# Optimization experiments

Hardware: AMD Instinct MI355X
Metric: run time of the kernel (lower is better)

The kernel has to match this reference:

```python
import jax, jax.numpy as jnp
import numpy as np
from jax import lax

DIM = 64
HEADS = 4
GN_EPS = 1e-5
L2_EPS = 1e-12


def conv2d(x, w, b=None, pad=0, groups=1, dil=1):
    out = lax.conv_general_dilated(
        x, w, window_strides=(1, 1), padding=[(pad, pad), (pad, pad)],
        rhs_dilation=(dil, dil), dimension_numbers=('NCHW', 'OIHW', 'NCHW'),
        feature_group_count=groups)
    if b is not None:
        out = out + b[None, :, None, None]
    return out


def group_norm2(x, gamma, beta):
    # GroupNorm with 2 groups over (C/2, H, W)
    b, c, h, w = x.shape
    xr = x.reshape(b, 2, c // 2, h, w)
    mu = xr.mean(axis=(2, 3, 4), keepdims=True)
    var = xr.var(axis=(2, 3, 4), keepdims=True)
    xn = ((xr - mu) * lax.rsqrt(var + GN_EPS)).reshape(b, c, h, w)
    return xn * gamma[None, :, None, None] + beta[None, :, None, None]


def lka(x, c0w, c0b, csw, csb, c1w, c1b, gn_g, gn_b):
    dim = c0w.shape[0]
    a = conv2d(x, c0w, c0b, pad=2, groups=dim)           # depthwise 5x5
    a = conv2d(a, csw, csb, pad=3, groups=dim, dil=3)    # depthwise 3x3, dilation 3
    a = conv2d(a, c1w, c1b, pad=0)                       # 1x1 pointwise
    return jax.nn.leaky_relu(group_norm2(a, gn_g, gn_b), 0.2)


def l2norm_lastdim(t):
    n = jnp.sqrt(jnp.sum(t * t, axis=-1, keepdims=True))
    return t / jnp.maximum(n, L2_EPS)


def setup_inputs() -> dict:
    key = jax.random.key(0)
    ks = jax.random.split(key, 24)
    B, C, H, W = 4, DIM, 256, 256
    s = 0.05

    def rn(k, shape, scale=s):
        return jax.random.normal(k, shape, dtype=jnp.float32) * scale

    d2 = 2 * DIM
    inp = {
        'x': jax.random.normal(ks[0], (B, C, H, W), dtype=jnp.float32),
        'y': jax.random.normal(ks[1], (B, C, H, W), dtype=jnp.float32),
        # 1x1 projections (bias=False)
        'kv_w': rn(ks[2], (d2, DIM, 1, 1)),
        'q_w': rn(ks[3], (DIM, DIM, 1, 1)),
        'proj_w': rn(ks[4], (DIM, DIM, 1, 1)),
        # kv LKA (C_hid = C_out = 128)
        'kv_c0_w': rn(ks[5], (d2, 1, 5, 5)), 'kv_c0_b': rn(ks[6], (d2,)),
        'kv_cs_w': rn(ks[7], (d2, 1, 3, 3)), 'kv_cs_b': rn(ks[8], (d2,)),
        'kv_c1_w': rn(ks[9], (d2, d2, 1, 1)), 'kv_c1_b': rn(ks[10], (d2,)),
        'kv_gn_g': jnp.ones((d2,), jnp.float32), 'kv_gn_b': jnp.zeros((d2,), jnp.float32),
        # q LKA (C_hid = C_out = 64)
        'q_c0_w': rn(ks[11], (DIM, 1, 5, 5)), 'q_c0_b': rn(ks[12], (DIM,)),
        'q_cs_w': rn(ks[13], (DIM, 1, 3, 3)), 'q_cs_b': rn(ks[14], (DIM,)),
        'q_c1_w': rn(ks[15], (DIM, DIM, 1, 1)), 'q_c1_b': rn(ks[16], (DIM,)),
        'q_gn_g': jnp.ones((DIM,), jnp.float32), 'q_gn_b': jnp.zeros((DIM,), jnp.float32),
        'temperature': jnp.ones((HEADS, 1, 1), jnp.float32),
    }
    return inp


def reference(x, y, kv_w, q_w, proj_w,
              kv_c0_w, kv_c0_b, kv_cs_w, kv_cs_b, kv_c1_w, kv_c1_b, kv_gn_g, kv_gn_b,
              q_c0_w, q_c0_b, q_cs_w, q_cs_b, q_c1_w, q_c1_b, q_gn_g, q_gn_b,
              temperature):
    b, c, h, w = x.shape
    kv = lka(conv2d(y, kv_w), kv_c0_w, kv_c0_b, kv_cs_w, kv_cs_b, kv_c1_w, kv_c1_b, kv_gn_g, kv_gn_b)
    k, v = jnp.split(kv, 2, axis=1)
    q = lka(conv2d(x, q_w), q_c0_w, q_c0_b, q_cs_w, q_cs_b, q_c1_w, q_c1_b, q_gn_g, q_gn_b)

    ch = c // HEADS
    hw = h * w
    q = q.reshape(b, HEADS, ch, hw)
    k = k.reshape(b, HEADS, ch, hw)
    v = v.reshape(b, HEADS, ch, hw)

    q = l2norm_lastdim(q)
    k = l2norm_lastdim(k)

    attn = jnp.einsum('bhcn,bhdn->bhcd', q, k) * temperature[None]  # [b,H,ch,ch]
    attn = jax.nn.softmax(attn, axis=-1)
    out = jnp.einsum('bhcd,bhdn->bhcn', attn, v).reshape(b, c, h, w)
    return conv2d(out, proj_w)
```

## Files before the change

### kernel.cpp

```cpp
#include <hip/hip_runtime.h>

#define HW 65536
#define IMG 256

__device__ __forceinline__ float hsum4(float4 v) { return v.x + v.y + v.z + v.w; }
__device__ __forceinline__ float lrelu(float v) { return v >= 0.f ? v : 0.2f * v; }

template<int CIT, int CO, bool GNIN, bool DUAL, bool INB, bool OUTB>
__global__ __launch_bounds__(CO*8)
void conv1x1_v7(const float* __restrict__ in, int in_cs, int in_coff,
                const float* __restrict__ in2, int in2_cs,
                const float* __restrict__ w, int w_bstride,
                const float* __restrict__ bias,
                float* __restrict__ out, int out_cs, int out_coff,
                float* __restrict__ stats, int gsel,
                const float* __restrict__ gstats,
                const float* __restrict__ g_gamma, const float* __restrict__ g_beta,
                int g_coff, float g_Nf)
{
    const int b  = blockIdx.y;
    const int T  = blockIdx.x;
    const int q  = threadIdx.x & 127;
    const int coh = __builtin_amdgcn_readfirstlane((int)(threadIdx.x >> 7));
    const int co0 = coh * 16;
    const float* wb = w + (size_t)b * w_bstride;

    float gmean = 0.f, grstd = 0.f;
    if (GNIN) {
        gmean = gstats[b*4] / g_Nf;
        float var = gstats[b*4 + 1] / g_Nf - gmean * gmean;
        grstd = rsqrtf(var + 1e-5f);
    }

    float4 acc[16];
    #pragma unroll
    for (int k = 0; k < 16; ++k) {
        float bv = bias ? bias[co0 + k] : 0.f;
        acc[k] = make_float4(bv, bv, bv, bv);
    }

    auto run = [&](const float4* t4, int cs, int coff, const float* wrb, int gci0, int n) {
        const float4* base = INB
            ? t4 + ((size_t)T * cs + coff) * 128 + q
            : t4 + (size_t)coff * (HW/4) + (size_t)T * 128 + q;
        const size_t cstr = INB ? 128 : (HW/4);
        #pragma unroll 4
        for (int ci = 0; ci < n; ++ci) {
            float4 x = base[(size_t)ci * cstr];
            if (GNIN) {
                float A = g_gamma[g_coff + gci0 + ci] * grstd;
                float B = g_beta[g_coff + gci0 + ci] - gmean * A;
                x.x = lrelu(fmaf(x.x, A, B));
                x.y = lrelu(fmaf(x.y, A, B));
                x.z = lrelu(fmaf(x.z, A, B));
                x.w = lrelu(fmaf(x.w, A, B));
            }
            const float* wr = wrb + gci0 + ci;
            #pragma unroll
            for (int k = 0; k < 16; ++k) {
                float wk = wr[(size_t)(co0 + k) * CIT];
                acc[k].x = fmaf(wk, x.x, acc[k].x);
                acc[k].y = fmaf(wk, x.y, acc[k].y);
                acc[k].z = fmaf(wk, x.z, acc[k].z);
                acc[k].w = fmaf(wk, x.w, acc[k].w);
            }
        }
    };

    const float4* inA = (const float4*)in + (size_t)b * in_cs * (HW/4);
    if (DUAL) {
        const float4* inB = (const float4*)in2 + (size_t)b * in2_cs * (HW/4);
        run(inA, in_cs, in_coff, wb, 0, 64);
        run(inB, in2_cs, 0, wb, 64, 64);
    } else {
        run(inA, in_cs, in_coff, wb, 0, CIT);
    }

    if (!GNIN && stats) {
        float s = 0.f, ss = 0.f;
        #pragma unroll
        for (int k = 0; k < 16; ++k) {
            s  += acc[k].x + acc[k].y + acc[k].z + acc[k].w;
            ss += acc[k].x*acc[k].x + acc[k].y*acc[k].y
                + acc[k].z*acc[k].z + acc[k].w*acc[k].w;
        }
        #pragma unroll
        for (int o = 32; o; o >>= 1) { s += __shfl_down(s, o, 64); ss += __shfl_down(ss, o, 64); }
        if ((threadIdx.x & 63) == 0) {
            int g = 0;
            if (gsel == -1) g = (co0 >= 32) ? 1 : 0;
            else if (gsel == -2) g = (co0 >= 64) ? 1 : 0;
            float* st = stats + (size_t)b*4 + g*2;
            atomicAdd(st,     s);
            atomicAdd(st + 1, ss);
        }
    }

    float4* ob = (float4*)out + (size_t)b * out_cs * (HW/4);
    #pragma unroll
    for (int k = 0; k < 16; ++k) {
        if (OUTB)
            ob[((size_t)T * out_cs + out_coff + co0 + k) * 128 + q] = acc[k];
        else
            ob[(size_t)(out_coff + co0 + k) * (HW/4) + (size_t)T * 128 + q] = acc[k];
    }
}

__global__ __launch_bounds__(256)
void dwfused(const float* __restrict__ in, int in_cs, int in_coff,
             const float* __restrict__ w5, const float* __restrict__ b5, int w5_coff,
             const float* __restrict__ w3, const float* __restrict__ b3, int w3_coff,
             float* __restrict__ out, int out_cs, int out_coff)
{
    constexpr int TH = 32, TW = 64;
    constexpr int IN_H = TH + 10, IN_W = TW + 10;
    constexpr int MID_H = TH + 6, MID_W = TW + 6;
    constexpr int IN_RS = IN_W + 2;
    constexpr int MID_RS = MID_W + 2;
    __shared__ float Xs[IN_H * IN_RS];
    __shared__ float Ms[MID_H * MID_RS];
    const int z = blockIdx.z;
    const int c = z & 63, b = z >> 6;
    const int x0 = blockIdx.x * TW, y0 = blockIdx.y * TH;
    const float* ib = in + (size_t)b * in_cs * HW;

    float wk5[25];
    #pragma unroll
    for (int i = 0; i < 25; ++i) wk5[i] = w5[(size_t)(w5_coff + c)*25 + i];
    const float bv5 = b5[w5_coff + c];
    float wk3[9];
    #pragma unroll
    for (int i = 0; i < 9; ++i) wk3[i] = w3[(size_t)(w3_coff + c)*9 + i];
    const float bv3 = b3[w3_coff + c];

    for (int idx = threadIdx.x; idx < IN_H*IN_W; idx += 256) {
        int ly = idx / IN_W, lx = idx - ly*IN_W;
        int gy = y0 + ly - 5, gx = x0 + lx - 5;
        float v = 0.f;
        if (gy >= 0 && gy < IMG && gx >= 0 && gx < IMG)
            v = ib[((size_t)(gy >> 1) * in_cs + in_coff + c) * 512 + (gy & 1) * 256 + gx];
        Xs[ly*IN_RS + lx] = v;
    }
    __syncthreads();

    for (int idx = threadIdx.x; idx < MID_H*MID_W; idx += 256) {
        int my = idx / MID_W, mx = idx - my*MID_W;
        int gy = y0 + my - 3, gx = x0 + mx - 3;
        float v = 0.f;
        if (gy >= 0 && gy < IMG && gx >= 0 && gx < IMG) {
            v = bv5;
            #pragma unroll
            for (int ky = 0; ky < 5; ++ky) {
                const float* xr = &Xs[(my + ky)*IN_RS + mx];
                #pragma unroll
                for (int kx = 0; kx < 5; ++kx)
                    v = fmaf(wk5[ky*5 + kx], xr[kx], v);
            }
        }
        Ms[my*MID_RS + mx] = v;
    }
    __syncthreads();

    const int qx = (threadIdx.x & 15) * 4;
    const int ly0 = threadIdx.x >> 4;
    float* ob = out + (size_t)b * out_cs * HW;
    #pragma unroll
    for (int r = 0; r < 2; ++r) {
        const int oy = ly0 + r*16;
        float o0 = bv3, o1 = bv3, o2 = bv3, o3 = bv3;
        #pragma unroll
        for (int kt = 0; kt < 3; ++kt) {
            const float* mr = &Ms[(oy + 3*kt)*MID_RS + qx];
            #pragma unroll
            for (int kx = 0; kx < 3; ++kx) {
                float wv_ = wk3[kt*3 + kx];
                o0 = fmaf(wv_, mr[3*kx + 0], o0);
                o1 = fmaf(wv_, mr[3*kx + 1], o1);
                o2 = fmaf(wv_, mr[3*kx + 2], o2);
                o3 = fmaf(wv_, mr[3*kx + 3], o3);
            }
        }
        const int y = y0 + oy;
        *(float4*)(ob + ((size_t)(y >> 1) * out_cs + out_coff + c) * 512 + (y & 1) * 256 + x0 + qx) =
            make_float4(o0, o1, o2, o3);
    }
}

__global__ __launch_bounds__(256)
void attn_dot_v5(const float* __restrict__ qt, int q_cs,
                 const float* __restrict__ kt, int k_cs,
                 const float* __restrict__ stQ, const float* __restrict__ stK,
                 const float* __restrict__ qg, const float* __restrict__ qb,
                 const float* __restrict__ kg, const float* __restrict__ kb,
                 float* __restrict__ attn_raw,
                 float* __restrict__ ssq, float* __restrict__ ssk)
{
    __shared__ float4 qs[2048], ks[2048];
    __shared__ float sred[512];
    const int h = blockIdx.y, b = blockIdx.z;
    const int T = blockIdx.x;
    const int cc = threadIdx.x & 15;
    const int ch = h*16 + cc;

    const int gq = (ch >= 32) ? 1 : 0;
    float mq = stQ[b*4 + gq*2] / (32.f * HW);
    float vq = stQ[b*4 + gq*2 + 1] / (32.f * HW) - mq*mq;
    const float Aq = qg[ch] * rsqrtf(vq + 1e-5f);
    const float Bq = qb[ch] - mq * Aq;
    float mk = stK[b*4] / (64.f * HW);
    float vk = stK[b*4 + 1] / (64.f * HW) - mk*mk;
    const float Ak = kg[ch] * rsqrtf(vk + 1e-5f);
    const float Bk = kb[ch] - mk * Ak;

    const float4* q4 = (const float4*)qt + (size_t)b*q_cs*(HW/4) + ((size_t)T*q_cs + ch)*128;
    const float4* k4 = (const float4*)kt + (size_t)b*k_cs*(HW/4) + ((size_t)T*k_cs + ch)*128;
    float sq_acc = 0.f, sk_acc = 0.f;
    #pragma unroll
    for (int s = 0; s < 8; ++s) {
        int t = (threadIdx.x >> 4) + s*16;
        float4 v = q4[t];
        v.x = lrelu(fmaf(v.x, Aq, Bq)); v.y = lrelu(fmaf(v.y, Aq, Bq));
        v.z = lrelu(fmaf(v.z, Aq, Bq)); v.w = lrelu(fmaf(v.w, Aq, Bq));
        sq_acc += v.x*v.x + v.y*v.y + v.z*v.z + v.w*v.w;
        qs[t*16 + cc] = v;
        float4 u = k4[t];
        u.x = lrelu(fmaf(u.x, Ak, Bk)); u.y = lrelu(fmaf(u.y, Ak, Bk));
        u.z = lrelu(fmaf(u.z, Ak, Bk)); u.w = lrelu(fmaf(u.w, Ak, Bk));
        sk_acc += u.x*u.x + u.y*u.y + u.z*u.z + u.w*u.w;
        ks[t*16 + cc] = u;
    }
    sred[threadIdx.x]       = sq_acc;
    sred[256 + threadIdx.x] = sk_acc;
    __syncthreads();

    const int p   = threadIdx.x & 63;
    const int sub = threadIdx.x >> 6;
    const int c0 = (p >> 3) << 1, d0 = (p & 7) << 1;
    float4 a00 = make_float4(0,0,0,0), a01 = a00, a10 = a00, a11 = a00;
    #pragma unroll
    for (int i = 0; i < 32; ++i) {
        int t = sub*32 + i;
        float4 qa = qs[t*16 + c0], qb_ = qs[t*16 + c0 + 1];
        float4 ka = ks[t*16 + d0], kb_ = ks[t*16 + d0 + 1];
        a00.x = fmaf(qa.x, ka.x, a00.x); a00.y = fmaf(qa.y, ka.y, a00.y);
        a00.z = fmaf(qa.z, ka.z, a00.z); a00.w = fmaf(qa.w, ka.w, a00.w);
        a01.x = fmaf(qa.x, kb_.x, a01.x); a01.y = fmaf(qa.y, kb_.y, a01.y);
        a01.z = fmaf(qa.z, kb_.z, a01.z); a01.w = fmaf(qa.w, kb_.w, a01.w);
        a10.x = fmaf(qb_.x, ka.x, a10.x); a10.y = fmaf(qb_.y, ka.y, a10.y);
        a10.z = fmaf(qb_.z, ka.z, a10.z); a10.w = fmaf(qb_.w, ka.w, a10.w);
        a11.x = fmaf(qb_.x, kb_.x, a11.x); a11.y = fmaf(qb_.y, kb_.y, a11.y);
        a11.z = fmaf(qb_.z, kb_.z, a11.z); a11.w = fmaf(qb_.w, kb_.w, a11.w);
    }
    float* ar = attn_raw + ((size_t)b*4 + h) * 256;
    atomicAdd(&ar[(c0  )*16 + d0  ], hsum4(a00));
    atomicAdd(&ar[(c0  )*16 + d0+1], hsum4(a01));
    atomicAdd(&ar[(c0+1)*16 + d0  ], hsum4(a10));
    atomicAdd(&ar[(c0+1)*16 + d0+1], hsum4(a11));

    if (threadIdx.x < 16) {
        float s = 0.f;
        #pragma unroll
        for (int jj = 0; jj < 16; ++jj) s += sred[threadIdx.x + 16*jj];
        atomicAdd(&ssq[b*64 + h*16 + threadIdx.x], s);
    } else if (threadIdx.x < 32) {
        const int c2 = threadIdx.x - 16;
        float s = 0.f;
        #pragma unroll
        for (int jj = 0; jj < 16; ++jj) s += sred[256 + c2 + 16*jj];
        atomicAdd(&ssk[b*64 + h*16 + c2], s);
    }
}

__global__ __launch_bounds__(256)
void attn_softmax_v2(const float* __restrict__ attn_raw,
                     const float* __restrict__ ssq, const float* __restrict__ ssk,
                     const float* __restrict__ temp, float* __restrict__ attn)
{
    const int h = blockIdx.x, b = blockIdx.y;
    const int c = threadIdx.x >> 4, d = threadIdx.x & 15;
    const float nq = fmaxf(sqrtf(ssq[b*64 + h*16 + c]), 1e-12f);
    const float nk = fmaxf(sqrtf(ssk[b*64 + h*16 + d]), 1e-12f);
    float logit = attn_raw[((size_t)b*4 + h)*256 + c*16 + d] / (nq * nk) * temp[h];
    float m = logit;
    #pragma unroll
    for (int o = 8; o; o >>= 1) m = fmaxf(m, __shfl_xor(m, o, 16));
    float e = expf(logit - m);
    float s = e;
    #pragma unroll
    for (int o = 8; o; o >>= 1) s += __shfl_xor(s, o, 16);
    attn[((size_t)b*4 + h)*256 + c*16 + d] = e / s;
}

__global__ __launch_bounds__(256)
void build_m_v2(const float* __restrict__ attn, const float* __restrict__ proj_w,
                float* __restrict__ M)
{
    const int b = blockIdx.x;
    for (int i = threadIdx.x; i < 4096; i += 256) {
        int co = i >> 6, ci = i & 63;
        int h = ci >> 4, d = ci & 15;
        float s = 0.f;
        #pragma unroll
        for (int cc = 0; cc < 16; ++cc)
            s += proj_w[co*64 + h*16 + cc] * attn[((size_t)b*4 + h)*256 + cc*16 + d];
        M[(size_t)b*4096 + i] = s;
    }
}

extern "C" void kernel_launch(void* const* d_in, const int* in_sizes, int n_in,
                              void* d_out, int out_size, void* d_ws, size_t ws_size,
                              hipStream_t stream)
{
    const float* x       = (const float*)d_in[0];
    const float* y       = (const float*)d_in[1];
    const float* kv_w    = (const float*)d_in[2];
    const float* q_w     = (const float*)d_in[3];
    const float* proj_w  = (const float*)d_in[4];
    const float* kv_c0_w = (const float*)d_in[5];
    const float* kv_c0_b = (const float*)d_in[6];
    const float* kv_cs_w = (const float*)d_in[7];
    const float* kv_cs_b = (const float*)d_in[8];
    const float* kv_c1_w = (const float*)d_in[9];
    const float* kv_c1_b = (const float*)d_in[10];
    const float* kv_gn_g = (const float*)d_in[11];
    const float* kv_gn_b = (const float*)d_in[12];
    const float* q_c0_w  = (const float*)d_in[13];
    const float* q_c0_b  = (const float*)d_in[14];
    const float* q_cs_w  = (const float*)d_in[15];
    const float* q_cs_b  = (const float*)d_in[16];
    const float* q_c1_w  = (const float*)d_in[17];
    const float* q_c1_b  = (const float*)d_in[18];
    const float* q_gn_g  = (const float*)d_in[19];
    const float* q_gn_b  = (const float*)d_in[20];
    const float* temp    = (const float*)d_in[21];

    float* ws       = (float*)d_ws;
    float* statsKV  = ws;
    float* statsQ   = ws + 16;
    float* sumsq_k  = ws + 32;
    float* sumsq_q  = ws + 288;
    float* attn_raw = ws + 544;
    float* attn     = ws + 4640;
    float* Mw       = ws + 8736;
    float* big      = (float*)((char*)d_ws + 131072);

    const size_t perb_bytes = (size_t)192 * HW * 4;
    int nb = 1;
    if      (ws_size >= 131072 + 4*perb_bytes) nb = 4;
    else if (ws_size >= 131072 + 2*perb_bytes) nb = 2;

    hipMemsetAsync(d_ws, 0, 102400, stream);
    dim3 blk(256);

    for (int b0 = 0; b0 < 4; b0 += nb) {
        const float* xb = x + (size_t)b0*64*HW;
        const float* yb = y + (size_t)b0*64*HW;
        float* H1 = big;
        float* H2 = big + (size_t)nb*128*HW;
        float* O  = (float*)d_out + (size_t)b0*64*HW;
        float* stK = statsKV + b0*4;
        float* stQ = statsQ  + b0*4;
        float* ssk = sumsq_k + b0*64;
        float* ssq = sumsq_q + b0*64;
        float* arw = attn_raw + b0*1024;
        float* atn = attn     + b0*1024;
        float* Mb  = Mw       + b0*4096;

        dim3 gdwf(4, 8, nb*64);
        dim3 gcv(128, nb);

        conv1x1_v7<64,128,false,false,false,true><<<gcv, dim3(1024), 0, stream>>>(
            yb, 64, 0, nullptr, 0, kv_w, 0, nullptr, H1, 128, 0,
            nullptr, 0, nullptr, nullptr, nullptr, 0, 0.f);
        dwfused<<<gdwf, blk, 0, stream>>>(H1, 128, 0,  kv_c0_w, kv_c0_b, 0,  kv_cs_w, kv_cs_b, 0,  H2, 64, 0);
        dwfused<<<gdwf, blk, 0, stream>>>(H1, 128, 64, kv_c0_w, kv_c0_b, 64, kv_cs_w, kv_cs_b, 64, O,  64, 0);
        conv1x1_v7<128,128,false,true,true,true><<<gcv, dim3(1024), 0, stream>>>(
            H2, 64, 0, O, 64, kv_c1_w, 0, kv_c1_b, H1, 128, 0,
            stK, -2, nullptr, nullptr, nullptr, 0, 0.f);

        conv1x1_v7<64,64,false,false,false,true><<<gcv, dim3(512), 0, stream>>>(
            xb, 64, 0, nullptr, 0, q_w, 0, nullptr, O, 64, 0,
            nullptr, 0, nullptr, nullptr, nullptr, 0, 0.f);
        dwfused<<<gdwf, blk, 0, stream>>>(O, 64, 0, q_c0_w, q_c0_b, 0, q_cs_w, q_cs_b, 0, H2, 64, 0);
        conv1x1_v7<64,64,false,false,true,true><<<gcv, dim3(512), 0, stream>>>(
            H2, 64, 0, nullptr, 0, q_c1_w, 0, q_c1_b, O, 64, 0,
            stQ, -1, nullptr, nullptr, nullptr, 0, 0.f);

        attn_dot_v5<<<dim3(128,4,nb), blk, 0, stream>>>(O, 64, H1, 128, stQ, stK,
                                                        q_gn_g, q_gn_b, kv_gn_g, kv_gn_b,
                                                        arw, ssq, ssk);
        attn_softmax_v2<<<dim3(4,nb), blk, 0, stream>>>(arw, ssq, ssk, temp, atn);
        build_m_v2<<<dim3(nb), blk, 0, stream>>>(atn, proj_w, Mb);

        conv1x1_v7<64,64,true,false,true,false><<<gcv, dim3(512), 0, stream>>>(
            H1, 128, 64, nullptr, 0, Mw + b0*4096, 4096, nullptr,
            (float*)d_out + (size_t)b0*64*HW, 64, 0,
            nullptr, 0, stK+2, kv_gn_g, kv_gn_b, 64, 64.f*HW);
    }
}
```

Measured before the change: 1.017 ms.

## Stage conv1x1 input tiles into LDS with async global_load_lds double buffering

New measurement: 1.164 ms. 14.4% more time.

```diff
diff --git a/kernel.cpp b/kernel.cpp
--- a/kernel.cpp
+++ b/kernel.cpp
@@ -6,9 +6,15 @@
 __device__ __forceinline__ float hsum4(float4 v) { return v.x + v.y + v.z + v.w; }
 __device__ __forceinline__ float lrelu(float v) { return v >= 0.f ? v : 0.2f * v; }
 
+typedef const __attribute__((address_space(1))) unsigned int guint;
+typedef __attribute__((address_space(3))) unsigned int luint;
+__device__ __forceinline__ void gload_lds16(const float4* g, float4* l) {
+    __builtin_amdgcn_global_load_lds((guint*)(const void*)g, (luint*)(void*)l, 16, 0, 0);
+}
+
 template<int CIT, int CO, bool GNIN, bool DUAL, bool INB, bool OUTB>
 __global__ __launch_bounds__(CO*8)
-void conv1x1_v7(const float* __restrict__ in, int in_cs, int in_coff,
+void conv1x1_v9(const float* __restrict__ in, int in_cs, int in_coff,
                 const float* __restrict__ in2, int in2_cs,
                 const float* __restrict__ w, int w_bstride,
                 const float* __restrict__ bias,
@@ -18,11 +24,19 @@
                 const float* __restrict__ g_gamma, const float* __restrict__ g_beta,
                 int g_coff, float g_Nf)
 {
-    const int b  = blockIdx.y;
-    const int T  = blockIdx.x;
-    const int q  = threadIdx.x & 127;
-    const int coh = __builtin_amdgcn_readfirstlane((int)(threadIdx.x >> 7));
-    const int co0 = coh * 16;
+    constexpr int CI_CHUNK = (CIT == 128) ? 32 : 16;
+    constexpr int NCHUNK   = CIT / CI_CHUNK;
+    constexpr int NW       = CO / 8;
+    constexpr int PPW      = CI_CHUNK * 2 / NW;
+    __shared__ float4 Xs[2][CI_CHUNK * 128];
+
+    const int b    = blockIdx.y;
+    const int T    = blockIdx.x;
+    const int q    = threadIdx.x & 127;
+    const int lane = threadIdx.x & 63;
+    const int wv   = __builtin_amdgcn_readfirstlane((int)(threadIdx.x >> 6));
+    const int coh  = __builtin_amdgcn_readfirstlane((int)(threadIdx.x >> 7));
+    const int co0  = coh * 16;
     const float* wb = w + (size_t)b * w_bstride;
 
     float gmean = 0.f, grstd = 0.f;
@@ -39,23 +53,43 @@
         acc[k] = make_float4(bv, bv, bv, bv);
     }
 
-    auto run = [&](const float4* t4, int cs, int coff, const float* wrb, int gci0, int n) {
-        const float4* base = INB
-            ? t4 + ((size_t)T * cs + coff) * 128 + q
-            : t4 + (size_t)coff * (HW/4) + (size_t)T * 128 + q;
-        const size_t cstr = INB ? 128 : (HW/4);
-        #pragma unroll 4
-        for (int ci = 0; ci < n; ++ci) {
-            float4 x = base[(size_t)ci * cstr];
+    const float4* inA = (const float4*)in + (size_t)b * in_cs * (HW/4);
+    const float4* inB = DUAL ? ((const float4*)in2 + (size_t)b * in2_cs * (HW/4)) : nullptr;
+
+    auto stage = [&](int ch, int bs) {
+        #pragma unroll
+        for (int u = 0; u < PPW; ++u) {
+            const int piece = wv * PPW + u;
+            const int lci   = piece >> 1;
+            const int half  = piece & 1;
+            const int gci   = ch * CI_CHUNK + lci;
+            const float4* src;
+            if (INB) {
+                if (DUAL && gci >= 64)
+                    src = inB + ((size_t)T * in2_cs + (gci - 64)) * 128 + half * 64 + lane;
+                else
+                    src = inA + ((size_t)T * in_cs + in_coff + gci) * 128 + half * 64 + lane;
+            } else {
+                src = inA + (size_t)(in_coff + gci) * (HW/4) + (size_t)(T*2 + half) * 64 + lane;
+            }
+            gload_lds16(src, &Xs[bs][lci * 128 + half * 64]);
+        }
+    };
+
+    auto compute = [&](int ch, int bs) {
+        #pragma unroll 8
+        for (int lci = 0; lci < CI_CHUNK; ++lci) {
+            const int gci = ch * CI_CHUNK + lci;
+            float4 x = Xs[bs][lci * 128 + q];
             if (GNIN) {
-                float A = g_gamma[g_coff + gci0 + ci] * grstd;
-                float B = g_beta[g_coff + gci0 + ci] - gmean * A;
+                float A = g_gamma[g_coff + gci] * grstd;
+                float B = g_beta[g_coff + gci] - gmean * A;
                 x.x = lrelu(fmaf(x.x, A, B));
                 x.y = lrelu(fmaf(x.y, A, B));
                 x.z = lrelu(fmaf(x.z, A, B));
                 x.w = lrelu(fmaf(x.w, A, B));
             }
-            const float* wr = wrb + gci0 + ci;
+            const float* wr = wb + gci;
             #pragma unroll
             for (int k = 0; k < 16; ++k) {
                 float wk = wr[(size_t)(co0 + k) * CIT];
@@ -67,13 +101,12 @@
         }
     };
 
-    const float4* inA = (const float4*)in + (size_t)b * in_cs * (HW/4);
-    if (DUAL) {
-        const float4* inB = (const float4*)in2 + (size_t)b * in2_cs * (HW/4);
-        run(inA, in_cs, in_coff, wb, 0, 64);
-        run(inB, in2_cs, 0, wb, 64, 64);
-    } else {
-        run(inA, in_cs, in_coff, wb, 0, CIT);
+    stage(0, 0);
+    #pragma unroll 1
+    for (int ch = 0; ch < NCHUNK; ++ch) {
+        __syncthreads();
+        if (ch + 1 < NCHUNK) stage(ch + 1, (ch + 1) & 1);
+        compute(ch, ch & 1);
     }
 
     if (!GNIN && stats) {
@@ -86,7 +119,7 @@
         }
         #pragma unroll
         for (int o = 32; o; o >>= 1) { s += __shfl_down(s, o, 64); ss += __shfl_down(ss, o, 64); }
-        if ((threadIdx.x & 63) == 0) {
+        if (lane == 0) {
             int g = 0;
             if (gsel == -1) g = (co0 >= 32) ? 1 : 0;
             else if (gsel == -2) g = (co0 >= 64) ? 1 : 0;
@@ -369,20 +402,20 @@
         dim3 gdwf(4, 8, nb*64);
         dim3 gcv(128, nb);
 
-        conv1x1_v7<64,128,false,false,false,true><<<gcv, dim3(1024), 0, stream>>>(
+        conv1x1_v9<64,128,false,false,false,true><<<gcv, dim3(1024), 0, stream>>>(
             yb, 64, 0, nullptr, 0, kv_w, 0, nullptr, H1, 128, 0,
             nullptr, 0, nullptr, nullptr, nullptr, 0, 0.f);
         dwfused<<<gdwf, blk, 0, stream>>>(H1, 128, 0,  kv_c0_w, kv_c0_b, 0,  kv_cs_w, kv_cs_b, 0,  H2, 64, 0);
         dwfused<<<gdwf, blk, 0, stream>>>(H1, 128, 64, kv_c0_w, kv_c0_b, 64, kv_cs_w, kv_cs_b, 64, O,  64, 0);
-        conv1x1_v7<128,128,false,true,true,true><<<gcv, dim3(1024), 0, stream>>>(
+        conv1x1_v9<128,128,false,true,true,true><<<gcv, dim3(1024), 0, stream>>>(
             H2, 64, 0, O, 64, kv_c1_w, 0, kv_c1_b, H1, 128, 0,
             stK, -2, nullptr, nullptr, nullptr, 0, 0.f);
 
-        conv1x1_v7<64,64,false,false,false,true><<<gcv, dim3(512), 0, stream>>>(
+        conv1x1_v9<64,64,false,false,false,true><<<gcv, dim3(512), 0, stream>>>(
             xb, 64, 0, nullptr, 0, q_w, 0, nullptr, O, 64, 0,
             nullptr, 0, nullptr, nullptr, nullptr, 0, 0.f);
         dwfused<<<gdwf, blk, 0, stream>>>(O, 64, 0, q_c0_w, q_c0_b, 0, q_cs_w, q_cs_b, 0, H2, 64, 0);
-        conv1x1_v7<64,64,false,false,true,true><<<gcv, dim3(512), 0, stream>>>(
+        conv1x1_v9<64,64,false,false,true,true><<<gcv, dim3(512), 0, stream>>>(
             H2, 64, 0, nullptr, 0, q_c1_w, 0, q_c1_b, O, 64, 0,
             stQ, -1, nullptr, nullptr, nullptr, 0, 0.f);
 
@@ -392,7 +425,7 @@
         attn_softmax_v2<<<dim3(4,nb), blk, 0, stream>>>(arw, ssq, ssk, temp, atn);
         build_m_v2<<<dim3(nb), blk, 0, stream>>>(atn, proj_w, Mb);
 
-        conv1x1_v7<64,64,true,false,true,false><<<gcv, dim3(512), 0, stream>>>(
+        conv1x1_v9<64,64,true,false,true,false><<<gcv, dim3(512), 0, stream>>>(
             H1, 128, 64, nullptr, 0, Mw + b0*4096, 4096, nullptr,
             (float*)d_out + (size_t)b0*64*HW, 64, 0,
             nullptr, 0, stK+2, kv_gn_g, kv_gn_b, 64, 64.f*HW);
```

## Store all intermediate activations in bf16 and drop dual-input conv path

Applied to the files above, without the earlier changes.

Result: faster. 928.3 us (-8.8%).

```diff
diff --git a/kernel.cpp b/kernel.cpp
--- a/kernel.cpp
+++ b/kernel.cpp
@@ -5,22 +5,36 @@
 
 __device__ __forceinline__ float hsum4(float4 v) { return v.x + v.y + v.z + v.w; }
 __device__ __forceinline__ float lrelu(float v) { return v >= 0.f ? v : 0.2f * v; }
-
-template<int CIT, int CO, bool GNIN, bool DUAL, bool INB, bool OUTB>
+__device__ __forceinline__ float bf2f(unsigned short u) {
+    return __uint_as_float(((unsigned)u) << 16);
+}
+__device__ __forceinline__ unsigned short f2bf(float f) {
+    unsigned i = __float_as_uint(f);
+    return (unsigned short)((i + 0x7FFFu + ((i >> 16) & 1u)) >> 16);
+}
+__device__ __forceinline__ float4 dq4(ushort4 u) {
+    return make_float4(bf2f(u.x), bf2f(u.y), bf2f(u.z), bf2f(u.w));
+}
+__device__ __forceinline__ ushort4 qz4(float4 v) {
+    ushort4 u; u.x = f2bf(v.x); u.y = f2bf(v.y); u.z = f2bf(v.z); u.w = f2bf(v.w);
+    return u;
+}
+
+template<int CIT, int CO, int INM, int OUTM, bool GNIN>
 __global__ __launch_bounds__(CO*8)
-void conv1x1_v7(const float* __restrict__ in, int in_cs, int in_coff,
-                const float* __restrict__ in2, int in2_cs,
-                const float* __restrict__ w, int w_bstride,
-                const float* __restrict__ bias,
-                float* __restrict__ out, int out_cs, int out_coff,
-                float* __restrict__ stats, int gsel,
-                const float* __restrict__ gstats,
-                const float* __restrict__ g_gamma, const float* __restrict__ g_beta,
-                int g_coff, float g_Nf)
-{
-    const int b  = blockIdx.y;
-    const int T  = blockIdx.x;
-    const int q  = threadIdx.x & 127;
+void conv1x1_v10(const void* __restrict__ in, int in_cs, int in_coff,
+                 const float* __restrict__ w, int w_bstride,
+                 const float* __restrict__ bias,
+                 void* __restrict__ out, int out_cs, int out_coff,
+                 float* __restrict__ stats, int gsel,
+                 const float* __restrict__ gstats,
+                 const float* __restrict__ g_gamma, const float* __restrict__ g_beta,
+                 int g_coff, float g_Nf)
+{
+    const int b   = blockIdx.y;
+    const int T   = blockIdx.x;
+    const int q   = threadIdx.x & 127;
+    const int lane = threadIdx.x & 63;
     const int coh = __builtin_amdgcn_readfirstlane((int)(threadIdx.x >> 7));
     const int co0 = coh * 16;
     const float* wb = w + (size_t)b * w_bstride;
@@ -39,41 +53,43 @@
         acc[k] = make_float4(bv, bv, bv, bv);
     }
 
-    auto run = [&](const float4* t4, int cs, int coff, const float* wrb, int gci0, int n) {
-        const float4* base = INB
-            ? t4 + ((size_t)T * cs + coff) * 128 + q
-            : t4 + (size_t)coff * (HW/4) + (size_t)T * 128 + q;
-        const size_t cstr = INB ? 128 : (HW/4);
-        #pragma unroll 4
-        for (int ci = 0; ci < n; ++ci) {
-            float4 x = base[(size_t)ci * cstr];
-            if (GNIN) {
-                float A = g_gamma[g_coff + gci0 + ci] * grstd;
-                float B = g_beta[g_coff + gci0 + ci] - gmean * A;
-                x.x = lrelu(fmaf(x.x, A, B));
-                x.y = lrelu(fmaf(x.y, A, B));
-                x.z = lrelu(fmaf(x.z, A, B));
-                x.w = lrelu(fmaf(x.w, A, B));
-            }
-            const float* wr = wrb + gci0 + ci;
-            #pragma unroll
-            for (int k = 0; k < 16; ++k) {
-                float wk = wr[(size_t)(co0 + k) * CIT];
-                acc[k].x = fmaf(wk, x.x, acc[k].x);
-                acc[k].y = fmaf(wk, x.y, acc[k].y);
-                acc[k].z = fmaf(wk, x.z, acc[k].z);
-                acc[k].w = fmaf(wk, x.w, acc[k].w);
-            }
-        }
-    };
-
-    const float4* inA = (const float4*)in + (size_t)b * in_cs * (HW/4);
-    if (DUAL) {
-        const float4* inB = (const float4*)in2 + (size_t)b * in2_cs * (HW/4);
-        run(inA, in_cs, in_coff, wb, 0, 64);
-        run(inB, in2_cs, 0, wb, 64, 64);
+    const float4*  bf4 = nullptr;
+    const ushort4* bu4 = nullptr;
+    size_t cstr;
+    if (INM == 0) {
+        bf4 = (const float4*)in + ((size_t)b * in_cs + in_coff) * (HW/4)
+            + (size_t)T * 128 + q;
+        cstr = HW/4;
+    } else if (INM == 1) {
+        bf4 = (const float4*)in + (size_t)b * in_cs * (HW/4)
+            + ((size_t)T * in_cs + in_coff) * 128 + q;
+        cstr = 128;
     } else {
-        run(inA, in_cs, in_coff, wb, 0, CIT);
+        bu4 = (const ushort4*)in + (size_t)b * in_cs * (HW/4)
+            + ((size_t)T * in_cs + in_coff) * 128 + q;
+        cstr = 128;
+    }
+
+    #pragma unroll 4
+    for (int ci = 0; ci < CIT; ++ci) {
+        float4 x = (INM == 2) ? dq4(bu4[(size_t)ci * cstr]) : bf4[(size_t)ci * cstr];
+        if (GNIN) {
+            float A = g_gamma[g_coff + ci] * grstd;
+            float B = g_beta[g_coff + ci] - gmean * A;
+            x.x = lrelu(fmaf(x.x, A, B));
+            x.y = lrelu(fmaf(x.y, A, B));
+            x.z = lrelu(fmaf(x.z, A, B));
+            x.w = lrelu(fmaf(x.w, A, B));
+        }
+        const float* wr = wb + ci;
+        #pragma unroll
+        for (int k = 0; k < 16; ++k) {
+            float wk = wr[(size_t)(co0 + k) * CIT];
+            acc[k].x = fmaf(wk, x.x, acc[k].x);
+            acc[k].y = fmaf(wk, x.y, acc[k].y);
+            acc[k].z = fmaf(wk, x.z, acc[k].z);
+            acc[k].w = fmaf(wk, x.w, acc[k].w);
+        }
     }
 
     if (!GNIN && stats) {
@@ -86,7 +102,7 @@
         }
         #pragma unroll
         for (int o = 32; o; o >>= 1) { s += __shfl_down(s, o, 64); ss += __shfl_down(ss, o, 64); }
-        if ((threadIdx.x & 63) == 0) {
+        if (lane == 0) {
             int g = 0;
             if (gsel == -1) g = (co0 >= 32) ? 1 : 0;
             else if (gsel == -2) g = (co0 >= 64) ? 1 : 0;
@@ -96,21 +112,24 @@
         }
     }
 
-    float4* ob = (float4*)out + (size_t)b * out_cs * (HW/4);
-    #pragma unroll
-    for (int k = 0; k < 16; ++k) {
-        if (OUTB)
-            ob[((size_t)T * out_cs + out_coff + co0 + k) * 128 + q] = acc[k];
-        else
+    if (OUTM == 0) {
+        float4* ob = (float4*)out + (size_t)b * out_cs * (HW/4);
+        #pragma unroll
+        for (int k = 0; k < 16; ++k)
             ob[(size_t)(out_coff + co0 + k) * (HW/4) + (size_t)T * 128 + q] = acc[k];
+    } else {
+        ushort4* ob = (ushort4*)out + (size_t)b * out_cs * (HW/4);
+        #pragma unroll
+        for (int k = 0; k < 16; ++k)
+            ob[((size_t)T * out_cs + out_coff + co0 + k) * 128 + q] = qz4(acc[k]);
     }
 }
 
 __global__ __launch_bounds__(256)
-void dwfused(const float* __restrict__ in, int in_cs, int in_coff,
-             const float* __restrict__ w5, const float* __restrict__ b5, int w5_coff,
-             const float* __restrict__ w3, const float* __restrict__ b3, int w3_coff,
-             float* __restrict__ out, int out_cs, int out_coff)
+void dwfused16(const unsigned short* __restrict__ in, int in_cs, int in_coff,
+               const float* __restrict__ w5, const float* __restrict__ b5, int w5_coff,
+               const float* __restrict__ w3, const float* __restrict__ b3, int w3_coff,
+               unsigned short* __restrict__ out, int out_cs, int out_coff)
 {
     constexpr int TH = 32, TW = 64;
     constexpr int IN_H = TH + 10, IN_W = TW + 10;
@@ -122,7 +141,7 @@
     const int z = blockIdx.z;
     const int c = z & 63, b = z >> 6;
     const int x0 = blockIdx.x * TW, y0 = blockIdx.y * TH;
-    const float* ib = in + (size_t)b * in_cs * HW;
+    const unsigned short* ib = in + (size_t)b * in_cs * HW;
 
     float wk5[25];
     #pragma unroll
@@ -138,7 +157,7 @@
         int gy = y0 + ly - 5, gx = x0 + lx - 5;
         float v = 0.f;
         if (gy >= 0 && gy < IMG && gx >= 0 && gx < IMG)
-            v = ib[((size_t)(gy >> 1) * in_cs + in_coff + c) * 512 + (gy & 1) * 256 + gx];
+            v = bf2f(ib[((size_t)(gy >> 1) * in_cs + in_coff + c) * 512 + (gy & 1) * 256 + gx]);
         Xs[ly*IN_RS + lx] = v;
     }
     __syncthreads();
@@ -163,7 +182,7 @@
 
     const int qx = (threadIdx.x & 15) * 4;
     const int ly0 = threadIdx.x >> 4;
-    float* ob = out + (size_t)b * out_cs * HW;
+    unsigned short* ob = out + (size_t)b * out_cs * HW;
     #pragma unroll
     for (int r = 0; r < 2; ++r) {
         const int oy = ly0 + r*16;
@@ -181,14 +200,14 @@
             }
         }
         const int y = y0 + oy;
-        *(float4*)(ob + ((size_t)(y >> 1) * out_cs + out_coff + c) * 512 + (y & 1) * 256 + x0 + qx) =
-            make_float4(o0, o1, o2, o3);
+        *(ushort4*)(ob + ((size_t)(y >> 1) * out_cs + out_coff + c) * 512 + (y & 1) * 256 + x0 + qx) =
+            qz4(make_float4(o0, o1, o2, o3));
     }
 }
 
 __global__ __launch_bounds__(256)
-void attn_dot_v5(const float* __restrict__ qt, int q_cs,
-                 const float* __restrict__ kt, int k_cs,
+void attn_dot_v6(const unsigned short* __restrict__ qt, int q_cs,
+                 const unsigned short* __restrict__ kt, int k_cs,
                  const float* __restrict__ stQ, const float* __restrict__ stK,
                  const float* __restrict__ qg, const float* __restrict__ qb,
                  const float* __restrict__ kg, const float* __restrict__ kb,
@@ -212,18 +231,18 @@
     const float Ak = kg[ch] * rsqrtf(vk + 1e-5f);
     const float Bk = kb[ch] - mk * Ak;
 
-    const float4* q4 = (const float4*)qt + (size_t)b*q_cs*(HW/4) + ((size_t)T*q_cs + ch)*128;
-    const float4* k4 = (const float4*)kt + (size_t)b*k_cs*(HW/4) + ((size_t)T*k_cs + ch)*128;
+    const ushort4* q4 = (const ushort4*)qt + (size_t)b*q_cs*(HW/4) + ((size_t)T*q_cs + ch)*128;
+    const ushort4* k4 = (const ushort4*)kt + (size_t)b*k_cs*(HW/4) + ((size_t)T*k_cs + ch)*128;
     float sq_acc = 0.f, sk_acc = 0.f;
     #pragma unroll
     for (int s = 0; s < 8; ++s) {
         int t = (threadIdx.x >> 4) + s*16;
-        float4 v = q4[t];
+        float4 v = dq4(q4[t]);
         v.x = lrelu(fmaf(v.x, Aq, Bq)); v.y = lrelu(fmaf(v.y, Aq, Bq));
         v.z = lrelu(fmaf(v.z, Aq, Bq)); v.w = lrelu(fmaf(v.w, Aq, Bq));
         sq_acc += v.x*v.x + v.y*v.y + v.z*v.z + v.w*v.w;
         qs[t*16 + cc] = v;
-        float4 u = k4[t];
+        float4 u = dq4(k4[t]);
         u.x = lrelu(fmaf(u.x, Ak, Bk)); u.y = lrelu(fmaf(u.y, Ak, Bk));
         u.z = lrelu(fmaf(u.z, Ak, Bk)); u.w = lrelu(fmaf(u.w, Ak, Bk));
         sk_acc += u.x*u.x + u.y*u.y + u.z*u.z + u.w*u.w;
@@ -342,7 +361,7 @@
     float* attn_raw = ws + 544;
     float* attn     = ws + 4640;
     float* Mw       = ws + 8736;
-    float* big      = (float*)((char*)d_ws + 131072);
+    char*  bigc     = (char*)d_ws + 131072;
 
     const size_t perb_bytes = (size_t)192 * HW * 4;
     int nb = 1;
@@ -355,9 +374,13 @@
     for (int b0 = 0; b0 < 4; b0 += nb) {
         const float* xb = x + (size_t)b0*64*HW;
         const float* yb = y + (size_t)b0*64*HW;
-        float* H1 = big;
-        float* H2 = big + (size_t)nb*128*HW;
-        float* O  = (float*)d_out + (size_t)b0*64*HW;
+        const size_t SZ = (size_t)nb * 128 * HW;
+        unsigned short* A  = (unsigned short*)bigc;
+        unsigned short* Bm = A + SZ;
+        unsigned short* C  = A + 2*SZ;
+        unsigned short* Q1 = A;
+        unsigned short* Q2 = A + (size_t)nb * 64 * HW;
+        unsigned short* QF = Bm;
         float* stK = statsKV + b0*4;
         float* stQ = statsQ  + b0*4;
         float* ssk = sumsq_k + b0*64;
@@ -369,31 +392,31 @@
         dim3 gdwf(4, 8, nb*64);
         dim3 gcv(128, nb);
 
-        conv1x1_v7<64,128,false,false,false,true><<<gcv, dim3(1024), 0, stream>>>(
-            yb, 64, 0, nullptr, 0, kv_w, 0, nullptr, H1, 128, 0,
+        conv1x1_v10<64,128, 0,2, false><<<gcv, dim3(1024), 0, stream>>>(
+            yb, 64, 0, kv_w, 0, nullptr, A, 128, 0,
             nullptr, 0, nullptr, nullptr, nullptr, 0, 0.f);
-        dwfused<<<gdwf, blk, 0, stream>>>(H1, 128, 0,  kv_c0_w, kv_c0_b, 0,  kv_cs_w, kv_cs_b, 0,  H2, 64, 0);
-        dwfused<<<gdwf, blk, 0, stream>>>(H1, 128, 64, kv_c0_w, kv_c0_b, 64, kv_cs_w, kv_cs_b, 64, O,  64, 0);
-        conv1x1_v7<128,128,false,true,true,true><<<gcv, dim3(1024), 0, stream>>>(
-            H2, 64, 0, O, 64, kv_c1_w, 0, kv_c1_b, H1, 128, 0,
+        dwfused16<<<gdwf, blk, 0, stream>>>(A, 128, 0,  kv_c0_w, kv_c0_b, 0,  kv_cs_w, kv_cs_b, 0,  Bm, 128, 0);
+        dwfused16<<<gdwf, blk, 0, stream>>>(A, 128, 64, kv_c0_w, kv_c0_b, 64, kv_cs_w, kv_cs_b, 64, Bm, 128, 64);
+        conv1x1_v10<128,128, 2,2, false><<<gcv, dim3(1024), 0, stream>>>(
+            Bm, 128, 0, kv_c1_w, 0, kv_c1_b, C, 128, 0,
             stK, -2, nullptr, nullptr, nullptr, 0, 0.f);
 
-        conv1x1_v7<64,64,false,false,false,true><<<gcv, dim3(512), 0, stream>>>(
-            xb, 64, 0, nullptr, 0, q_w, 0, nullptr, O, 64, 0,
+        conv1x1_v10<64,64, 0,2, false><<<gcv, dim3(512), 0, stream>>>(
+            xb, 64, 0, q_w, 0, nullptr, Q1, 64, 0,
             nullptr, 0, nullptr, nullptr, nullptr, 0, 0.f);
-        dwfused<<<gdwf, blk, 0, stream>>>(O, 64, 0, q_c0_w, q_c0_b, 0, q_cs_w, q_cs_b, 0, H2, 64, 0);
-        conv1x1_v7<64,64,false,false,true,true><<<gcv, dim3(512), 0, stream>>>(
-            H2, 64, 0, nullptr, 0, q_c1_w, 0, q_c1_b, O, 64, 0,
+        dwfused16<<<gdwf, blk, 0, stream>>>(Q1, 64, 0, q_c0_w, q_c0_b, 0, q_cs_w, q_cs_b, 0, Q2, 64, 0);
+        conv1x1_v10<64,64, 2,2, false><<<gcv, dim3(512), 0, stream>>>(
+            Q2, 64, 0, q_c1_w, 0, q_c1_b, QF, 64, 0,
             stQ, -1, nullptr, nullptr, nullptr, 0, 0.f);
 
-        attn_dot_v5<<<dim3(128,4,nb), blk, 0, stream>>>(O, 64, H1, 128, stQ, stK,
+        attn_dot_v6<<<dim3(128,4,nb), blk, 0, stream>>>(QF, 64, C, 128, stQ, stK,
                                                         q_gn_g, q_gn_b, kv_gn_g, kv_gn_b,
                                                         arw, ssq, ssk);
         attn_softmax_v2<<<dim3(4,nb), blk, 0, stream>>>(arw, ssq, ssk, temp, atn);
         build_m_v2<<<dim3(nb), blk, 0, stream>>>(atn, proj_w, Mb);
 
-        conv1x1_v7<64,64,true,false,true,false><<<gcv, dim3(512), 0, stream>>>(
-            H1, 128, 64, nullptr, 0, Mw + b0*4096, 4096, nullptr,
+        conv1x1_v10<64,64, 2,0, true><<<gcv, dim3(512), 0, stream>>>(
+            C, 128, 64, Mw + b0*4096, 4096, nullptr,
             (float*)d_out + (size_t)b0*64*HW, 64, 0,
             nullptr, 0, stK+2, kv_gn_g, kv_gn_b, 64, 64.f*HW);
     }
```
